# Performance work log

Measured on AMD Instinct MI355X. Metric: run time of the kernel, lower is better.

The kernel has to match this reference:

```python
import jax, jax.numpy as jnp
import numpy as np

B, S, D, H = 4, 2048, 1024, 16
DH = D // H
SCALE = float(np.sqrt(DH))


def setup_inputs() -> dict:
    key = jax.random.key(0)
    ks = jax.random.split(key, 5)
    std = 1.0 / np.sqrt(D)
    return {
        "x": jax.random.normal(ks[0], (B, S, D), dtype=jnp.float32),
        "Wq": jax.random.normal(ks[1], (D, D), dtype=jnp.float32) * std,
        "bq": jnp.zeros((D,), dtype=jnp.float32),
        "Wk": jax.random.normal(ks[2], (D, D), dtype=jnp.float32) * std,
        "bk": jnp.zeros((D,), dtype=jnp.float32),
        "Wv": jax.random.normal(ks[3], (D, D), dtype=jnp.float32) * std,
        "bv": jnp.zeros((D,), dtype=jnp.float32),
        "Wo": jax.random.normal(ks[4], (D, D), dtype=jnp.float32) * std,
        "bo": jnp.zeros((D,), dtype=jnp.float32),
        "padding_mask": jnp.ones((B, S), dtype=jnp.int32),
    }


def reference(x, Wq, bq, Wk, bk, Wv, bv, Wo, bo, padding_mask):
    b, s, d = x.shape
    # QKV projections, split heads -> [b, h, s, dh]
    q = (x @ Wq + bq).reshape(b, s, H, DH).transpose(0, 2, 1, 3)
    k = (x @ Wk + bk).reshape(b, s, H, DH).transpose(0, 2, 1, 3)
    v = (x @ Wv + bv).reshape(b, s, H, DH).transpose(0, 2, 1, 3)
    # scaled scores [b, h, s, s]
    scores = jnp.einsum('bhqd,bhkd->bhqk', q, k) / SCALE
    neg_inf = jnp.float32(-jnp.inf)
    causal = jnp.tril(jnp.ones((s, s), dtype=bool))  # [s, s]
    scores = jnp.where(causal[None, None, :, :], scores, neg_inf)
    pad = (padding_mask != 0)[:, None, None, :]  # [b,1,1,s] on key axis
    scores = jnp.where(pad, scores, neg_inf)
    weights = jax.nn.softmax(scores, axis=-1)
    weights = jnp.nan_to_num(weights, nan=0.0)  # fully-masked rows -> 0
    # dropout is identity in eval / p=0
    attended = jnp.einsum('bhqk,bhkd->bhqd', weights, v)
    attended = attended.transpose(0, 2, 1, 3).reshape(b, s, d)
    return attended @ Wo + bo
```

## Files before the change

### kernel.cpp

```cpp
#include <hip/hip_runtime.h>
#include <hip/hip_bf16.h>

#define B_   4
#define S_   2048
#define D_   1024
#define H_   16
#define DH_  64
#define M_   (B_ * S_)

typedef __attribute__((ext_vector_type(8))) short  bfrag8;
typedef __attribute__((ext_vector_type(4))) float  facc4;
typedef unsigned short u16;
typedef unsigned long long u64;

__device__ __forceinline__ u16 f2bf(float f) {
    union { __hip_bfloat16 h; u16 u; } c;
    c.h = __float2bfloat16(f);
    return c.u;
}

__device__ __forceinline__ u16 bfr(float f) {
    unsigned b = __float_as_uint(f);
    return (u16)((b + 0x7FFFu + ((b >> 16) & 1u)) >> 16);
}

__device__ __forceinline__ void gl_lds16(const u16* g, u16* l) {
    __builtin_amdgcn_global_load_lds((const __attribute__((address_space(1))) void*)g,
                                     (__attribute__((address_space(3))) void*)l,
                                     16, 0, 0);
}

__global__ __launch_bounds__(256) void cvt_x(const float* __restrict__ x,
                                             u16* __restrict__ o, int n) {
    int i = (blockIdx.x * 256 + threadIdx.x) * 4;
    if (i >= n) return;
    float4 v = *(const float4*)(x + i);
    ushort4 r;
    r.x = f2bf(v.x); r.y = f2bf(v.y); r.z = f2bf(v.z); r.w = f2bf(v.w);
    *(ushort4*)(o + i) = r;
}

__global__ __launch_bounds__(256) void cvt_wt(const float* __restrict__ w0, const float* __restrict__ w1,
                                              const float* __restrict__ w2, const float* __restrict__ w3,
                                              u16* __restrict__ o0, u16* __restrict__ o1,
                                              u16* __restrict__ o2, u16* __restrict__ o3) {
    const float* w; u16* o;
    switch (blockIdx.z) {
        case 0: w = w0; o = o0; break;
        case 1: w = w1; o = o1; break;
        case 2: w = w2; o = o2; break;
        default: w = w3; o = o3; break;
    }
    __shared__ u16 t[32][33];
    int kb = blockIdx.x * 32, nb = blockIdx.y * 32;
    int c = threadIdx.x & 31, r0 = threadIdx.x >> 5;
#pragma unroll
    for (int i = 0; i < 4; i++) {
        int r = r0 + 8 * i;
        t[r][c] = f2bf(w[(kb + r) * D_ + nb + c]);
    }
    __syncthreads();
#pragma unroll
    for (int i = 0; i < 4; i++) {
        int r = r0 + 8 * i;
        o[(nb + r) * D_ + kb + c] = t[c][r];
    }
}

__global__ __launch_bounds__(64) void pack_pm(const int* __restrict__ pm,
                                              unsigned* __restrict__ pmw) {
    int b = blockIdx.x, lane = threadIdx.x;
#pragma unroll
    for (int j = 0; j < 32; ++j) {
        u64 m = __ballot(pm[b * S_ + j * 64 + lane] != 0);
        if (lane == 0) {
            pmw[b * 64 + 2 * j]     = (unsigned)m;
            pmw[b * 64 + 2 * j + 1] = (unsigned)(m >> 32);
        }
    }
}

#define ABUF_ (256 * 64)
#define TBUF_ ((256 + 128) * 64)

__device__ __forceinline__ void gemm_body256(const u16* __restrict__ A,
                                             const u16* __restrict__ BT,
                                             const float* __restrict__ bias,
                                             void* __restrict__ Cout, int mode, float scale,
                                             u16* S, int nb, int mb) {
    int tid = threadIdx.x;
    int w = tid >> 6, lane = tid & 63, quad = lane >> 4, l16 = lane & 15;
    int wm = (w >> 1) * 64, wn = (w & 1) * 64;
    int x7 = l16 & 7;

    const u16* Aga[4]; const u16* Bga[2];
#pragma unroll
    for (int i = 0; i < 4; ++i) {
        int idx = i * 512 + tid, row = idx >> 3;
        int lu = (idx & 7) ^ (row & 7);
        Aga[i] = A + (size_t)(mb + row) * D_ + lu * 8;
    }
#pragma unroll
    for (int i = 0; i < 2; ++i) {
        int idx = i * 512 + tid, row = idx >> 3;
        int lu = (idx & 7) ^ (row & 7);
        Bga[i] = BT + (size_t)(nb + row) * D_ + lu * 8;
    }

    facc4 acc[4][4] = {};

#pragma unroll
    for (int i = 0; i < 4; ++i) gl_lds16(Aga[i], S + (i * 512 + tid) * 8);
#pragma unroll
    for (int i = 0; i < 2; ++i) gl_lds16(Bga[i], S + ABUF_ + (i * 512 + tid) * 8);
    asm volatile("s_waitcnt vmcnt(0)" ::: "memory");
    __builtin_amdgcn_sched_barrier(0);
    __builtin_amdgcn_s_barrier();
    __builtin_amdgcn_sched_barrier(0);

    for (int kt = 0; kt < 16; ++kt) {
        u16* Cb = S + (kt & 1) * TBUF_;
        u16* Nb = S + ((kt & 1) ^ 1) * TBUF_;
        if (kt < 15) {
            int ko = (kt + 1) * 64;
#pragma unroll
            for (int i = 0; i < 4; ++i) gl_lds16(Aga[i] + ko, Nb + (i * 512 + tid) * 8);
#pragma unroll
            for (int i = 0; i < 2; ++i) gl_lds16(Bga[i] + ko, Nb + ABUF_ + (i * 512 + tid) * 8);
        }
#pragma unroll
        for (int k2 = 0; k2 < 2; ++k2) {
            int pu = ((k2 * 4 + quad) ^ x7) * 8;
            bfrag8 af[4], bf[4];
#pragma unroll
            for (int mt = 0; mt < 4; ++mt)
                af[mt] = *(const bfrag8*)(Cb + (wm + mt * 16 + l16) * 64 + pu);
#pragma unroll
            for (int nt = 0; nt < 4; ++nt)
                bf[nt] = *(const bfrag8*)(Cb + ABUF_ + (wn + nt * 16 + l16) * 64 + pu);
            __builtin_amdgcn_s_setprio(1);
#pragma unroll
            for (int mt = 0; mt < 4; ++mt)
#pragma unroll
                for (int nt = 0; nt < 4; ++nt)
                    acc[mt][nt] = __builtin_amdgcn_mfma_f32_16x16x32_bf16(af[mt], bf[nt], acc[mt][nt], 0, 0, 0);
            __builtin_amdgcn_s_setprio(0);
        }
        asm volatile("s_waitcnt vmcnt(0)" ::: "memory");
        __builtin_amdgcn_sched_barrier(0);
        __builtin_amdgcn_s_barrier();
        __builtin_amdgcn_sched_barrier(0);
    }

#pragma unroll
    for (int mt = 0; mt < 4; ++mt) {
        int m_base = mb + wm + mt * 16 + quad * 4;
#pragma unroll
        for (int nt = 0; nt < 4; ++nt) {
            int n = nb + wn + nt * 16 + l16;
            float bv = bias[n];
            int h = n >> 6, dd = n & 63;
#pragma unroll
            for (int r = 0; r < 4; ++r) {
                int m = m_base + r;
                float v = (acc[mt][nt][r] + bv) * scale;
                int bi = m >> 11, s = m & (S_ - 1);
                if (mode == 0) {
                    ((u16*)Cout)[(((bi * H_ + h) * S_) + s) * DH_ + dd] = bfr(v);
                } else if (mode == 1) {
                    ((u16*)Cout)[(((bi * H_ + h) * DH_) + dd) * S_ + s] = bfr(v);
                } else {
                    ((float*)Cout)[(size_t)m * D_ + n] = v;
                }
            }
        }
    }
}

#define CE_Q 0.18033688011112042f

__global__ __launch_bounds__(512, 2) void gemm_qkv(const u16* __restrict__ A,
                                                const u16* __restrict__ WTq, const float* __restrict__ bq, u16* __restrict__ Qb,
                                                const u16* __restrict__ WTk, const float* __restrict__ bk, u16* __restrict__ Kb,
                                                const u16* __restrict__ WTv, const float* __restrict__ bv, u16* __restrict__ VTb) {
    __shared__ __attribute__((aligned(16))) u16 Sh[2 * TBUF_];
    int lid = blockIdx.x;
    int xcd = lid & 7, s = lid >> 3;
    int z = s >> 5, inner = s & 31;
    int mb = (xcd * 4 + (inner >> 3)) * 256;
    int nb = (inner & 7) * 128;
    switch (z) {
        case 0: gemm_body256(A, WTq, bq, Qb, 0, CE_Q, Sh, nb, mb); break;
        case 1: gemm_body256(A, WTk, bk, Kb, 0, 1.0f, Sh, nb, mb); break;
        default: gemm_body256(A, WTv, bv, VTb, 1, 1.0f, Sh, nb, mb); break;
    }
}

__global__ __launch_bounds__(512, 2) void gemm_o(const u16* __restrict__ A,
                                              const u16* __restrict__ WTo, const float* __restrict__ bo,
                                              float* __restrict__ out) {
    __shared__ __attribute__((aligned(16))) u16 Sh[2 * TBUF_];
    int lid = blockIdx.x;
    int xcd = lid & 7, s = lid >> 3;
    int mb = (xcd * 4 + (s >> 3)) * 256;
    int nb = (s & 7) * 128;
    gemm_body256(A, WTo, bo, out, 2, 1.0f, Sh, nb, mb);
}

__device__ __forceinline__ void soft_pv(const float* p, float& lp, facc4* oaccq,
                                        const bfrag8* vf, int a0, int a1, bool qlo) {
    float rs = 0.f;
    unsigned pk[4];
#pragma unroll
    for (int j = 0; j < 4; ++j) {
        float e0 = exp2f(p[2 * j]);
        float e1 = exp2f(p[2 * j + 1]);
        rs += e0; rs += e1;
        pk[j] = __builtin_amdgcn_perm(__float_as_uint(e1), __float_as_uint(e0), 0x07060302u);
    }
    lp += rs;
    union { unsigned d[4]; bfrag8 v; } pb;
    {
        unsigned lo, hi;
        lo = __builtin_amdgcn_ds_bpermute(a0, (int)pk[0]);
        hi = __builtin_amdgcn_ds_bpermute(a0, (int)pk[2]);
        pb.d[0] = qlo ? lo : hi;
        lo = __builtin_amdgcn_ds_bpermute(a0, (int)pk[1]);
        hi = __builtin_amdgcn_ds_bpermute(a0, (int)pk[3]);
        pb.d[1] = qlo ? lo : hi;
        lo = __builtin_amdgcn_ds_bpermute(a1, (int)pk[0]);
        hi = __builtin_amdgcn_ds_bpermute(a1, (int)pk[2]);
        pb.d[2] = qlo ? lo : hi;
        lo = __builtin_amdgcn_ds_bpermute(a1, (int)pk[1]);
        hi = __builtin_amdgcn_ds_bpermute(a1, (int)pk[3]);
        pb.d[3] = qlo ? lo : hi;
    }
    __builtin_amdgcn_s_setprio(1);
#pragma unroll
    for (int dt = 0; dt < 4; ++dt)
        oaccq[dt] = __builtin_amdgcn_mfma_f32_16x16x32_bf16(vf[dt], pb.v, oaccq[dt], 0, 0, 0);
    __builtin_amdgcn_s_setprio(0);
}

__global__ __launch_bounds__(256, 4) void attn(const u16* __restrict__ Q,
                                               const u16* __restrict__ K,
                                               const u16* __restrict__ VT,
                                               const unsigned* __restrict__ pmw,
                                               u16* __restrict__ Aout) {
    __shared__ __attribute__((aligned(16))) u16 Ks[32 * 64];
    __shared__ __attribute__((aligned(16))) u16 Vs[64 * 32];

    int tid = threadIdx.x, w = tid >> 6, lane = tid & 63;
    int quad = lane >> 4, l16 = lane & 15;

    int lid = blockIdx.x;
    int bh  = (lid & 7) * 8 + ((lid >> 3) & 7);
    int ci  = 15 - (lid >> 6);
    int b = bh >> 4, h = bh & 15;

    int qbase = ci * 128;
    int qw = qbase + w * 32;
    int tmax = (qbase >> 5) + 3;

    const u16* Qp = Q + (size_t)(b * H_ + h) * S_ * DH_;
    const u16* Kp = K + (size_t)(b * H_ + h) * S_ * DH_;
    const u16* Vp = VT + (size_t)(b * H_ + h) * DH_ * S_;
    const unsigned* pmb = pmw + b * 64;
    u16* Ao = Aout + (size_t)b * S_ * D_ + h * DH_;

    int krow = tid >> 3, ku = tid & 7;
    const u16* Kg = Kp + krow * DH_ + ((ku ^ (krow & 7)) * 8);
    u16* Kl = Ks + tid * 8;
    int vrow = tid >> 2, vu = tid & 3;
    const u16* Vg = Vp + vrow * S_ + ((vu ^ (vrow & 3)) * 8);
    u16* Vl = Vs + tid * 8;

    int k7 = l16 & 7, v3 = l16 & 3;

    int a0 = ((((2 * quad) & 3) * 16 + l16) << 2);
    int a1 = ((((2 * quad + 1) & 3) * 16 + l16) << 2);
    bool qlo = quad < 2;

    bfrag8 qf[2][2];
#pragma unroll
    for (int qt = 0; qt < 2; ++qt)
#pragma unroll
        for (int cc = 0; cc < 2; ++cc)
            qf[qt][cc] = *(const bfrag8*)(Qp + (qw + qt * 16 + l16) * DH_ + cc * 32 + quad * 8);

    facc4 oacc[2][4] = {};
    float lp[2] = {0.f, 0.f};

    for (int t = 0; t <= tmax; ++t) {
        int k0 = t * 32;
        __syncthreads();
        gl_lds16(Kg + k0 * DH_, Kl);
        gl_lds16(Vg + k0, Vl);
        __syncthreads();

        bfrag8 kf00 = *(const bfrag8*)(Ks + (l16 * 8        + ((quad)     ^ k7)) * 8);
        bfrag8 kf01 = *(const bfrag8*)(Ks + (l16 * 8        + ((quad + 4) ^ k7)) * 8);
        bfrag8 kf10 = *(const bfrag8*)(Ks + ((l16 + 16) * 8 + ((quad)     ^ k7)) * 8);
        bfrag8 kf11 = *(const bfrag8*)(Ks + ((l16 + 16) * 8 + ((quad + 4) ^ k7)) * 8);
        bfrag8 vf[4];
#pragma unroll
        for (int dt = 0; dt < 4; ++dt)
            vf[dt] = *(const bfrag8*)(Vs + ((dt * 16 + l16) * 4 + (quad ^ v3)) * 8);

        unsigned vm = pmb[t];

        facc4 st[2][2] = {};
        __builtin_amdgcn_s_setprio(1);
#pragma unroll
        for (int qt = 0; qt < 2; ++qt) {
            st[qt][0] = __builtin_amdgcn_mfma_f32_16x16x32_bf16(kf00, qf[qt][0], st[qt][0], 0, 0, 0);
            st[qt][0] = __builtin_amdgcn_mfma_f32_16x16x32_bf16(kf01, qf[qt][1], st[qt][0], 0, 0, 0);
            st[qt][1] = __builtin_amdgcn_mfma_f32_16x16x32_bf16(kf10, qf[qt][0], st[qt][1], 0, 0, 0);
            st[qt][1] = __builtin_amdgcn_mfma_f32_16x16x32_bf16(kf11, qf[qt][1], st[qt][1], 0, 0, 0);
        }
        __builtin_amdgcn_s_setprio(0);

        if (vm == 0xffffffffu && k0 + 31 < qw) {
#pragma unroll
            for (int qt = 0; qt < 2; ++qt) {
                float p[8];
#pragma unroll
                for (int kt = 0; kt < 2; ++kt)
#pragma unroll
                    for (int r = 0; r < 4; ++r) p[kt * 4 + r] = st[qt][kt][r];
                soft_pv(p, lp[qt], oacc[qt], vf, a0, a1, qlo);
            }
        } else {
#pragma unroll
            for (int qt = 0; qt < 2; ++qt) {
                int q0 = qw + qt * 16;
                float p[8];
#pragma unroll
                for (int kt = 0; kt < 2; ++kt)
#pragma unroll
                    for (int r = 0; r < 4; ++r) {
                        int kl = kt * 16 + quad * 4 + r;
                        bool ok = ((vm >> kl) & 1u) && (k0 + kl <= q0 + l16);
                        p[kt * 4 + r] = ok ? st[qt][kt][r] : -1e30f;
                    }
                soft_pv(p, lp[qt], oacc[qt], vf, a0, a1, qlo);
            }
        }
    }

#pragma unroll
    for (int qt = 0; qt < 2; ++qt) {
        float l = lp[qt];
        l += __shfl_xor(l, 16);
        l += __shfl_xor(l, 32);
        float linv = (l > 0.f) ? 1.f / l : 0.f;
        size_t qoff = (size_t)(qw + qt * 16 + l16) * D_;
#pragma unroll
        for (int dt = 0; dt < 4; ++dt) {
            union { u16 hh[4]; u64 q; } pk4;
#pragma unroll
            for (int r = 0; r < 4; ++r) pk4.hh[r] = bfr(oacc[qt][dt][r] * linv);
            *(u64*)(Ao + qoff + dt * 16 + quad * 4) = pk4.q;
        }
    }
}

extern "C" void kernel_launch(void* const* d_in, const int* in_sizes, int n_in,
                              void* d_out, int out_size, void* d_ws, size_t ws_size,
                              hipStream_t stream) {
    const float* x  = (const float*)d_in[0];
    const float* Wq = (const float*)d_in[1];
    const float* bq = (const float*)d_in[2];
    const float* Wk = (const float*)d_in[3];
    const float* bk = (const float*)d_in[4];
    const float* Wv = (const float*)d_in[5];
    const float* bv = (const float*)d_in[6];
    const float* Wo = (const float*)d_in[7];
    const float* bo = (const float*)d_in[8];
    const int*   pm = (const int*)d_in[9];
    float* out = (float*)d_out;

    char* ws = (char*)d_ws;
    const size_t SZ_XD = (size_t)M_ * D_ * 2;
    const size_t SZ_W  = (size_t)D_ * D_ * 2;
    u16* X16 = (u16*)ws;
    u16* WTq = (u16*)(ws + SZ_XD);
    u16* WTk = (u16*)(ws + SZ_XD + SZ_W);
    u16* WTv = (u16*)(ws + SZ_XD + 2 * SZ_W);
    u16* WTo = (u16*)(ws + SZ_XD + 3 * SZ_W);
    u16* Qb  = (u16*)(ws + SZ_XD + 4 * SZ_W);
    u16* Kb  = (u16*)(ws + 2 * SZ_XD + 4 * SZ_W);
    u16* VTb = (u16*)(ws + 3 * SZ_XD + 4 * SZ_W);
    u16* Att = X16;
    unsigned* PMW = (unsigned*)WTq;

    cvt_x<<<(M_ * D_) / (256 * 4), 256, 0, stream>>>(x, X16, M_ * D_);
    cvt_wt<<<dim3(D_ / 32, D_ / 32, 4), 256, 0, stream>>>(Wq, Wk, Wv, Wo, WTq, WTk, WTv, WTo);

    gemm_qkv<<<dim3(768), 512, 0, stream>>>(X16, WTq, bq, Qb, WTk, bk, Kb, WTv, bv, VTb);

    pack_pm<<<4, 64, 0, stream>>>(pm, PMW);

    attn<<<dim3(1024), 256, 0, stream>>>(Qb, Kb, VTb, PMW, Att);

    gemm_o<<<dim3(256), 512, 0, stream>>>(Att, WTo, bo, out);
}
```

Baseline: 279.3 us.

## Double-buffer K/V tiles in LDS and interleave causal chunk scheduling

The attention kernel now keeps two LDS buffers for the K and V tiles and prefetches the next tile while the current one is computed, which cuts one of the two barriers per iteration. This is meant to hide global-to-LDS latency behind the MFMA and softmax work. Block-to-query-chunk mapping also changes from a straight descending order to an interleaved order of heavy and light causal chunks, to balance work across waves of blocks. The cost is double the LDS footprint per block, which may limit occupancy at launch bounds of 4 blocks per CU.

```diff
diff --git a/kernel.cpp b/kernel.cpp
--- a/kernel.cpp
+++ b/kernel.cpp
@@ -247,15 +247,17 @@
                                                const u16* __restrict__ VT,
                                                const unsigned* __restrict__ pmw,
                                                u16* __restrict__ Aout) {
-    __shared__ __attribute__((aligned(16))) u16 Ks[32 * 64];
-    __shared__ __attribute__((aligned(16))) u16 Vs[64 * 32];
+    __shared__ __attribute__((aligned(16))) u16 Ks[2][32 * 64];
+    __shared__ __attribute__((aligned(16))) u16 Vs[2][64 * 32];
 
     int tid = threadIdx.x, w = tid >> 6, lane = tid & 63;
     int quad = lane >> 4, l16 = lane & 15;
 
     int lid = blockIdx.x;
     int bh  = (lid & 7) * 8 + ((lid >> 3) & 7);
-    int ci  = 15 - (lid >> 6);
+    int g   = lid >> 6;
+    int gq = g >> 2, gr = g & 3;
+    int ci = (gq == 0) ? 15 - gr : (gq == 1) ? gr : (gq == 2) ? 11 - gr : 4 + gr;
     int b = bh >> 4, h = bh & 15;
 
     int qbase = ci * 128;
@@ -270,10 +272,10 @@
 
     int krow = tid >> 3, ku = tid & 7;
     const u16* Kg = Kp + krow * DH_ + ((ku ^ (krow & 7)) * 8);
-    u16* Kl = Ks + tid * 8;
     int vrow = tid >> 2, vu = tid & 3;
     const u16* Vg = Vp + vrow * S_ + ((vu ^ (vrow & 3)) * 8);
-    u16* Vl = Vs + tid * 8;
+    u16* Kl[2] = { &Ks[0][tid * 8], &Ks[1][tid * 8] };
+    u16* Vl[2] = { &Vs[0][tid * 8], &Vs[1][tid * 8] };
 
     int k7 = l16 & 7, v3 = l16 & 3;
 
@@ -291,23 +293,32 @@
     facc4 oacc[2][4] = {};
     float lp[2] = {0.f, 0.f};
 
+    gl_lds16(Kg, Kl[0]);
+    gl_lds16(Vg, Vl[0]);
+    unsigned vmn = pmb[0];
+    __syncthreads();
+
     for (int t = 0; t <= tmax; ++t) {
+        int cur = t & 1, nxt = cur ^ 1;
+        unsigned vm = vmn;
+        if (t < tmax) {
+            int k1 = (t + 1) * 32;
+            gl_lds16(Kg + k1 * DH_, Kl[nxt]);
+            gl_lds16(Vg + k1, Vl[nxt]);
+            vmn = pmb[t + 1];
+        }
         int k0 = t * 32;
-        __syncthreads();
-        gl_lds16(Kg + k0 * DH_, Kl);
-        gl_lds16(Vg + k0, Vl);
-        __syncthreads();
-
-        bfrag8 kf00 = *(const bfrag8*)(Ks + (l16 * 8        + ((quad)     ^ k7)) * 8);
-        bfrag8 kf01 = *(const bfrag8*)(Ks + (l16 * 8        + ((quad + 4) ^ k7)) * 8);
-        bfrag8 kf10 = *(const bfrag8*)(Ks + ((l16 + 16) * 8 + ((quad)     ^ k7)) * 8);
-        bfrag8 kf11 = *(const bfrag8*)(Ks + ((l16 + 16) * 8 + ((quad + 4) ^ k7)) * 8);
+        const u16* Kc = Ks[cur];
+        const u16* Vc = Vs[cur];
+
+        bfrag8 kf00 = *(const bfrag8*)(Kc + (l16 * 8        + ((quad)     ^ k7)) * 8);
+        bfrag8 kf01 = *(const bfrag8*)(Kc + (l16 * 8        + ((quad + 4) ^ k7)) * 8);
+        bfrag8 kf10 = *(const bfrag8*)(Kc + ((l16 + 16) * 8 + ((quad)     ^ k7)) * 8);
+        bfrag8 kf11 = *(const bfrag8*)(Kc + ((l16 + 16) * 8 + ((quad + 4) ^ k7)) * 8);
         bfrag8 vf[4];
 #pragma unroll
         for (int dt = 0; dt < 4; ++dt)
-            vf[dt] = *(const bfrag8*)(Vs + ((dt * 16 + l16) * 4 + (quad ^ v3)) * 8);
-
-        unsigned vm = pmb[t];
+            vf[dt] = *(const bfrag8*)(Vc + ((dt * 16 + l16) * 4 + (quad ^ v3)) * 8);
 
         facc4 st[2][2] = {};
         __builtin_amdgcn_s_setprio(1);
@@ -346,6 +357,7 @@
                 soft_pv(p, lp[qt], oacc[qt], vf, a0, a1, qlo);
             }
         }
+        __syncthreads();
     }
 
 #pragma unroll
```

Result: faster. 268.2 us (-4.0%).
